# Kernel tuning notes

Hardware: AMD Instinct MI355X
Metric: run time of the kernel (lower is better)

## Reference

```python
import jax, jax.numpy as jnp
import numpy as np

INPUT_SIZE = 40960
HIDDEN = 256
BATCH = 16384
FEATS_PER_SAMPLE = 32


def _bag_sum(W, idx, offsets, num_segments):
    # EmbeddingBag(mode='sum'): segment ids from CSR offsets
    seg = jnp.searchsorted(offsets, jnp.arange(idx.shape[0]), side='right') - 1
    return jax.ops.segment_sum(W[idx], seg, num_segments=num_segments)


def setup_inputs() -> dict:
    key = jax.random.key(0)
    ks = jax.random.split(key, 12)
    n = BATCH * FEATS_PER_SAMPLE
    white_indices = jax.random.randint(ks[0], (n,), 0, INPUT_SIZE)
    black_indices = jax.random.randint(ks[1], (n,), 0, INPUT_SIZE)
    offsets = jnp.arange(BATCH, dtype=jnp.int64) * FEATS_PER_SAMPLE
    stm = (jax.random.uniform(ks[2], (BATCH, 1)) > 0.5).astype(jnp.float32)
    s_ft = 1.0 / np.sqrt(HIDDEN)
    ft_w = jax.random.uniform(ks[3], (INPUT_SIZE, HIDDEN), minval=-s_ft, maxval=s_ft)
    ft_b = jnp.zeros((HIDDEN,), jnp.float32)
    s1 = 1.0 / np.sqrt(2 * HIDDEN)
    l1_w = jax.random.uniform(ks[4], (32, 2 * HIDDEN), minval=-s1, maxval=s1)
    l1_b = jax.random.uniform(ks[5], (32,), minval=-s1, maxval=s1)
    s2 = 1.0 / np.sqrt(32)
    l2_w = jax.random.uniform(ks[6], (32, 32), minval=-s2, maxval=s2)
    l2_b = jax.random.uniform(ks[7], (32,), minval=-s2, maxval=s2)
    l3_w = jax.random.uniform(ks[8], (1, 32), minval=-s2, maxval=s2)
    l3_b = jax.random.uniform(ks[9], (1,), minval=-s2, maxval=s2)
    return {
        'white_indices': white_indices, 'white_offsets': offsets,
        'black_indices': black_indices, 'black_offsets': offsets,
        'stm': stm,
        'ft_w': ft_w, 'ft_b': ft_b,
        'l1_w': l1_w, 'l1_b': l1_b,
        'l2_w': l2_w, 'l2_b': l2_b,
        'l3_w': l3_w, 'l3_b': l3_b,
    }


def reference(white_indices, white_offsets, black_indices, black_offsets, stm,
              ft_w, ft_b, l1_w, l1_b, l2_w, l2_b, l3_w, l3_b):
    B = stm.shape[0]
    wh = jnp.clip(_bag_sum(ft_w, white_indices, white_offsets, B) + ft_b, 0.0, 1.0)
    bh = jnp.clip(_bag_sum(ft_w, black_indices, black_offsets, B) + ft_b, 0.0, 1.0)
    stm_b = stm.astype(bool)  # (B,1)
    hidden = jnp.where(stm_b,
                       jnp.concatenate([wh, bh], axis=-1),
                       jnp.concatenate([bh, wh], axis=-1))  # (B, 512)
    x = jnp.clip(hidden @ l1_w.T + l1_b, 0.0, 1.0)
    x = jnp.clip(x @ l2_w.T + l2_b, 0.0, 1.0)
    return x @ l3_w.T + l3_b  # (B, 1)
```

## Files before the change

### kernel.cpp

```cpp
#include <hip/hip_runtime.h>
#include <hip/hip_bf16.h>

#define NBATCH 16384
#define WPB 4
#define BLOCK 256

typedef unsigned int u32;
typedef unsigned char u8;

#define ENC 2032.0f
#define DEC 4.92125984e-4f
#define BIAS_SUM (4096.0f * DEC)

__device__ __forceinline__ float clamp01(float x){ return fminf(fmaxf(x, 0.f), 1.f); }

template<int D>
__device__ __forceinline__ float lane_xor_f(float x) {
    if constexpr (D == 1)
        return __int_as_float(__builtin_amdgcn_update_dpp(
            0, __float_as_int(x), 0xB1 , 0xF, 0xF, true));
    else if constexpr (D == 2)
        return __int_as_float(__builtin_amdgcn_update_dpp(
            0, __float_as_int(x), 0x4E , 0xF, 0xF, true));
    else
        return __shfl_xor(x, D, 64);
}

template<int D>
__device__ __forceinline__ void rs_stage(float (&p)[32], int lane) {
    const int mb = lane & D;
    #pragma unroll
    for (int j = 0; j < D; ++j) {
        float a = p[j], b = p[j + D];
        float snd = mb ? a : b;
        float kp  = mb ? b : a;
        p[j] = kp + lane_xor_f<D>(snd);
    }
}

__global__ __launch_bounds__(256) void convert_ftw_u8(
    const float* __restrict__ src, u32* __restrict__ dst, int n4)
{
    int i = blockIdx.x * blockDim.x + threadIdx.x;
    const int stride = gridDim.x * blockDim.x;
    for (; i < n4; i += stride) {
        float4 v = ((const float4*)src)[i];
        int q0 = __float2int_rn(v.x * ENC) + 128;
        int q1 = __float2int_rn(v.y * ENC) + 128;
        int q2 = __float2int_rn(v.z * ENC) + 128;
        int q3 = __float2int_rn(v.w * ENC) + 128;
        q0 = max(0, min(255, q0)); q1 = max(0, min(255, q1));
        q2 = max(0, min(255, q2)); q3 = max(0, min(255, q3));
        dst[i] = (u32)q0 | ((u32)q1 << 8) | ((u32)q2 << 16) | ((u32)q3 << 24);
    }
}

__global__ __launch_bounds__(BLOCK, 4) void nnue_fwd_u8tab(
    const int* __restrict__ wi, const int* __restrict__ bi,
    const float* __restrict__ stm,
    const u8* __restrict__ tab, const float* __restrict__ ftb,
    const float* __restrict__ l1w, const float* __restrict__ l1b,
    const float* __restrict__ l2w, const float* __restrict__ l2b,
    const float* __restrict__ l3w, const float* __restrict__ l3b,
    float* __restrict__ out)
{
    __shared__ __align__(16) float l1w_s[16*512];
    __shared__ __align__(16) float x1_s[WPB][32];
    __shared__ int idx_s[WPB][64];

    const int tid  = threadIdx.x;
    const int lane = tid & 63;
    const int wv   = tid >> 6;
    const int s    = blockIdx.x * WPB + wv;

    {
        const float4* src = (const float4*)l1w;
        #pragma unroll
        for (int i = 0; i < 8; ++i) {
            int j = tid + i*BLOCK;
            int B = j * 16;
            int W = B ^ ((B >> 3) & 16);
            *(float4*)((char*)l1w_s + W) = src[j];
        }
    }
    {
        int bse = s*32 + (lane & 31);
        idx_s[wv][lane] = (lane < 32) ? wi[bse] : bi[bse];
    }
    const bool wf = stm[s] > 0.5f;
    __syncthreads();

    const int chunk = lane & 31;
    const int hsel  = lane & 32;

    u32 sA = 0, sB = 0, sC = 0, sD = 0;
    #pragma unroll 8
    for (int j = 0; j < 32; ++j) {
        int row = idx_s[wv][j + hsel];
        uint2 w = *(const uint2*)(tab + (size_t)row*256 + chunk*8);
        sA += (w.x      ) & 0x00FF00FFu;
        sB += (w.x >> 8 ) & 0x00FF00FFu;
        sC += (w.y      ) & 0x00FF00FFu;
        sD += (w.y >> 8 ) & 0x00FF00FFu;
    }
    float acc[8];
    {
        float4 a = *(const float4*)(ftb + chunk*8);
        float4 b = *(const float4*)(ftb + chunk*8 + 4);
        acc[0] = fmaf((float)(sA & 0xFFFFu), DEC, a.x - BIAS_SUM);
        acc[1] = fmaf((float)(sB & 0xFFFFu), DEC, a.y - BIAS_SUM);
        acc[2] = fmaf((float)(sA >> 16    ), DEC, a.z - BIAS_SUM);
        acc[3] = fmaf((float)(sB >> 16    ), DEC, a.w - BIAS_SUM);
        acc[4] = fmaf((float)(sC & 0xFFFFu), DEC, b.x - BIAS_SUM);
        acc[5] = fmaf((float)(sD & 0xFFFFu), DEC, b.y - BIAS_SUM);
        acc[6] = fmaf((float)(sC >> 16    ), DEC, b.z - BIAS_SUM);
        acc[7] = fmaf((float)(sD >> 16    ), DEC, b.w - BIAS_SUM);
    }
    #pragma unroll
    for (int k = 0; k < 8; ++k) acc[k] = clamp01(acc[k]);

    const int wl    = wf ? lane : (lane ^ 32);
    const int wbyte = wl * 32;

    float p[32];
    #pragma unroll
    for (int o = 0; o < 16; ++o) {
        int b  = o*2048 + wbyte;
        int sw = b ^ ((b >> 3) & 16);
        float4 wa = *(const float4*)((const char*)l1w_s + sw);
        float4 wb = *(const float4*)((const char*)l1w_s + (sw ^ 16));
        p[o] = acc[0]*wa.x + acc[1]*wa.y + acc[2]*wa.z + acc[3]*wa.w
             + acc[4]*wb.x + acc[5]*wb.y + acc[6]*wb.z + acc[7]*wb.w;
    }
    __syncthreads();

    {
        const float4* src = (const float4*)l1w;
        #pragma unroll
        for (int i = 0; i < 8; ++i) {
            int j = tid + i*BLOCK;
            int B = j * 16;
            int W = B ^ ((B >> 3) & 16);
            *(float4*)((char*)l1w_s + W) = src[2048 + j];
        }
    }
    __syncthreads();

    const int j2 = lane & 31;
    float4 w2[8];
    {
        const float4* l2p = (const float4*)(l2w + j2*32);
        #pragma unroll
        for (int i = 0; i < 8; ++i) w2[i] = l2p[i];
    }
    const float l1b_r = l1b[j2];
    const float l2b_r = l2b[j2];
    const float l3w_r = l3w[j2];

    #pragma unroll
    for (int o = 0; o < 16; ++o) {
        int b  = o*2048 + wbyte;
        int sw = b ^ ((b >> 3) & 16);
        float4 wa = *(const float4*)((const char*)l1w_s + sw);
        float4 wb = *(const float4*)((const char*)l1w_s + (sw ^ 16));
        p[16+o] = acc[0]*wa.x + acc[1]*wa.y + acc[2]*wa.z + acc[3]*wa.w
                + acc[4]*wb.x + acc[5]*wb.y + acc[6]*wb.z + acc[7]*wb.w;
    }

    rs_stage<16>(p, lane);
    rs_stage<8 >(p, lane);
    rs_stage<4 >(p, lane);
    rs_stage<2 >(p, lane);
    rs_stage<1 >(p, lane);
    float psum = p[0] + __shfl_xor(p[0], 32, 64);

    float x1 = clamp01(psum + l1b_r);
    if (lane < 32) x1_s[wv][lane] = x1;

    const float4* xs = (const float4*)x1_s[wv];
    float a2 = l2b_r;
    #pragma unroll
    for (int i = 0; i < 8; ++i) {
        float4 xv = xs[i];
        a2 += xv.x*w2[i].x + xv.y*w2[i].y + xv.z*w2[i].z + xv.w*w2[i].w;
    }
    float x2 = clamp01(a2);

    float r = x2 * l3w_r;
    #pragma unroll
    for (int d = 16; d >= 1; d >>= 1) r += __shfl_xor(r, d, 64);

    if (lane == 0) out[s] = r + l3b[0];
}

__global__ __launch_bounds__(256, 4) void nnue_fwd_f32(
    const int* __restrict__ wi, const int* __restrict__ bi,
    const float* __restrict__ stm,
    const float* __restrict__ ftw, const float* __restrict__ ftb,
    const float* __restrict__ l1w, const float* __restrict__ l1b,
    const float* __restrict__ l2w, const float* __restrict__ l2b,
    const float* __restrict__ l3w, const float* __restrict__ l3b,
    float* __restrict__ out)
{
    __shared__ __align__(16) float l1w_s[16*512];
    __shared__ float l2w_s[32*33];
    __shared__ float l1b_s[32], l2b_s[32], l3w_s[32];
    __shared__ int idx_s[4][64];

    const int tid  = threadIdx.x;
    const int lane = tid & 63;
    const int wv   = tid >> 6;
    const int s    = blockIdx.x * 4 + wv;

    {
        const float4* src = (const float4*)l1w;
        float4* dst = (float4*)l1w_s;
        #pragma unroll
        for (int i = 0; i < 8; ++i) dst[tid + i*256] = src[tid + i*256];
    }
    for (int i = tid; i < 1024; i += 256)
        l2w_s[(i >> 5)*33 + (i & 31)] = l2w[i];
    if (tid < 32) {
        l1b_s[tid] = l1b[tid];
        l2b_s[tid] = l2b[tid];
        l3w_s[tid] = l3w[tid];
    }
    {
        int bse = s*32 + (lane & 31);
        idx_s[wv][lane] = (lane < 32) ? wi[bse] : bi[bse];
    }
    __syncthreads();

    const int chunk = lane & 31;
    const int hsel  = lane & 32;

    float acc[8];
    {
        float4 a = *(const float4*)(ftb + chunk*8);
        float4 b = *(const float4*)(ftb + chunk*8 + 4);
        acc[0]=a.x; acc[1]=a.y; acc[2]=a.z; acc[3]=a.w;
        acc[4]=b.x; acc[5]=b.y; acc[6]=b.z; acc[7]=b.w;
    }
    #pragma unroll 8
    for (int j = 0; j < 32; ++j) {
        int row = idx_s[wv][j + hsel];
        const float* rp = ftw + (size_t)row*256 + chunk*8;
        float4 a = *(const float4*)rp;
        float4 b = *(const float4*)(rp + 4);
        acc[0]+=a.x; acc[1]+=a.y; acc[2]+=a.z; acc[3]+=a.w;
        acc[4]+=b.x; acc[5]+=b.y; acc[6]+=b.z; acc[7]+=b.w;
    }
    #pragma unroll
    for (int k = 0; k < 8; ++k) acc[k] = clamp01(acc[k]);

    const bool wf = stm[s] > 0.5f;
    float h[8];
    #pragma unroll
    for (int k = 0; k < 8; ++k) {
        float x = __shfl_xor(acc[k], 32, 64);
        h[k] = wf ? acc[k] : x;
    }

    float p[32];
    #pragma unroll
    for (int o = 0; o < 16; ++o) {
        float4 wa = *(const float4*)&l1w_s[o*512 + lane*8];
        float4 wb = *(const float4*)&l1w_s[o*512 + lane*8 + 4];
        p[o] = h[0]*wa.x + h[1]*wa.y + h[2]*wa.z + h[3]*wa.w
             + h[4]*wb.x + h[5]*wb.y + h[6]*wb.z + h[7]*wb.w;
    }
    __syncthreads();
    {
        const float4* src = (const float4*)l1w;
        float4* dst = (float4*)l1w_s;
        #pragma unroll
        for (int i = 0; i < 8; ++i) dst[tid + i*256] = src[2048 + tid + i*256];
    }
    __syncthreads();
    #pragma unroll
    for (int o = 0; o < 16; ++o) {
        float4 wa = *(const float4*)&l1w_s[o*512 + lane*8];
        float4 wb = *(const float4*)&l1w_s[o*512 + lane*8 + 4];
        p[16+o] = h[0]*wa.x + h[1]*wa.y + h[2]*wa.z + h[3]*wa.w
                + h[4]*wb.x + h[5]*wb.y + h[6]*wb.z + h[7]*wb.w;
    }
    #pragma unroll
    for (int o = 0; o < 32; ++o) {
        #pragma unroll
        for (int d = 1; d < 64; d <<= 1)
            p[o] += __shfl_xor(p[o], d, 64);
    }
    float x1[32];
    #pragma unroll
    for (int o = 0; o < 32; ++o) x1[o] = clamp01(p[o] + l1b_s[o]);

    const int j2 = lane & 31;
    float a2 = l2b_s[j2];
    #pragma unroll
    for (int i = 0; i < 32; ++i) a2 += x1[i] * l2w_s[j2*33 + i];
    float x2 = clamp01(a2);

    float r = x2 * l3w_s[j2];
    #pragma unroll
    for (int d = 16; d >= 1; d >>= 1) r += __shfl_xor(r, d, 64);

    if (lane == 0) out[s] = r + l3b[0];
}

extern "C" void kernel_launch(void* const* d_in, const int* in_sizes, int n_in,
                              void* d_out, int out_size, void* d_ws, size_t ws_size,
                              hipStream_t stream)
{
    const int*   wi  = (const int*)d_in[0];
    const int*   bi  = (const int*)d_in[2];
    const float* stm = (const float*)d_in[4];
    const float* ftw = (const float*)d_in[5];
    const float* ftb = (const float*)d_in[6];
    const float* l1w = (const float*)d_in[7];
    const float* l1b = (const float*)d_in[8];
    const float* l2w = (const float*)d_in[9];
    const float* l2b = (const float*)d_in[10];
    const float* l3w = (const float*)d_in[11];
    const float* l3b = (const float*)d_in[12];

    const size_t tab_elems = (size_t)40960 * 256;
    const size_t need = tab_elems * sizeof(u8);
    if (ws_size >= need) {
        u8* tab = (u8*)d_ws;
        convert_ftw_u8<<<dim3(4096), dim3(256), 0, stream>>>(
            ftw, (u32*)tab, (int)(tab_elems / 4));
        nnue_fwd_u8tab<<<dim3(NBATCH / WPB), dim3(BLOCK), 0, stream>>>(
            wi, bi, stm, tab, ftb, l1w, l1b, l2w, l2b, l3w, l3b,
            (float*)d_out);
    } else {
        nnue_fwd_f32<<<dim3(NBATCH / 4), dim3(256), 0, stream>>>(
            wi, bi, stm, ftw, ftb, l1w, l1b, l2w, l2b, l3w, l3b,
            (float*)d_out);
    }
}
```

Before: 156.4 us.

## Halve L1 weight LDS tile and stage in four passes for higher occupancy

The shared l1 weight buffer shrinks from 32KB to 16KB and is refilled in four passes of 8 outputs instead of two passes of 16. Launch bounds rise to 8 blocks per CU. The layer-2 weights are no longer held in registers but read lazily from global memory, and the gather address math is simplified to 32-bit. This targets more resident waves to hide gather latency, at the cost of extra barriers and global reloads of l1 weights per block.

```diff
diff --git a/kernel.cpp b/kernel.cpp
--- a/kernel.cpp
+++ b/kernel.cpp
@@ -55,7 +55,7 @@
     }
 }
 
-__global__ __launch_bounds__(BLOCK, 4) void nnue_fwd_u8tab(
+__global__ __launch_bounds__(BLOCK, 8) void nnue_fwd_u8tab(
     const int* __restrict__ wi, const int* __restrict__ bi,
     const float* __restrict__ stm,
     const u8* __restrict__ tab, const float* __restrict__ ftb,
@@ -64,7 +64,7 @@
     const float* __restrict__ l3w, const float* __restrict__ l3b,
     float* __restrict__ out)
 {
-    __shared__ __align__(16) float l1w_s[16*512];
+    __shared__ __align__(16) float l1w_s[8*512];
     __shared__ __align__(16) float x1_s[WPB][32];
     __shared__ int idx_s[WPB][64];
 
@@ -76,11 +76,10 @@
     {
         const float4* src = (const float4*)l1w;
         #pragma unroll
-        for (int i = 0; i < 8; ++i) {
+        for (int i = 0; i < 4; ++i) {
             int j = tid + i*BLOCK;
             int B = j * 16;
-            int W = B ^ ((B >> 3) & 16);
-            *(float4*)((char*)l1w_s + W) = src[j];
+            *(float4*)((char*)l1w_s + (B ^ ((B >> 3) & 16))) = src[j];
         }
     }
     {
@@ -92,12 +91,13 @@
 
     const int chunk = lane & 31;
     const int hsel  = lane & 32;
+    const u32 coff  = (u32)chunk * 8u;
 
     u32 sA = 0, sB = 0, sC = 0, sD = 0;
     #pragma unroll 8
     for (int j = 0; j < 32; ++j) {
-        int row = idx_s[wv][j + hsel];
-        uint2 w = *(const uint2*)(tab + (size_t)row*256 + chunk*8);
+        u32 row = (u32)idx_s[wv][j + hsel];
+        uint2 w = *(const uint2*)(tab + ((row << 8) + coff));
         sA += (w.x      ) & 0x00FF00FFu;
         sB += (w.x >> 8 ) & 0x00FF00FFu;
         sC += (w.y      ) & 0x00FF00FFu;
@@ -121,51 +121,42 @@
 
     const int wl    = wf ? lane : (lane ^ 32);
     const int wbyte = wl * 32;
+    const int swb   = wbyte ^ ((wbyte >> 3) & 16);
+    const char* lbase  = (const char*)l1w_s + swb;
+    const char* lbase2 = (const char*)l1w_s + (swb ^ 16);
 
     float p[32];
     #pragma unroll
-    for (int o = 0; o < 16; ++o) {
-        int b  = o*2048 + wbyte;
-        int sw = b ^ ((b >> 3) & 16);
-        float4 wa = *(const float4*)((const char*)l1w_s + sw);
-        float4 wb = *(const float4*)((const char*)l1w_s + (sw ^ 16));
-        p[o] = acc[0]*wa.x + acc[1]*wa.y + acc[2]*wa.z + acc[3]*wa.w
-             + acc[4]*wb.x + acc[5]*wb.y + acc[6]*wb.z + acc[7]*wb.w;
-    }
-    __syncthreads();
-
-    {
-        const float4* src = (const float4*)l1w;
-        #pragma unroll
-        for (int i = 0; i < 8; ++i) {
-            int j = tid + i*BLOCK;
-            int B = j * 16;
-            int W = B ^ ((B >> 3) & 16);
-            *(float4*)((char*)l1w_s + W) = src[2048 + j];
+    for (int ol = 0; ol < 8; ++ol) {
+        float4 wa = *(const float4*)(lbase  + ol*2048);
+        float4 wb = *(const float4*)(lbase2 + ol*2048);
+        p[ol] = acc[0]*wa.x + acc[1]*wa.y + acc[2]*wa.z + acc[3]*wa.w
+              + acc[4]*wb.x + acc[5]*wb.y + acc[6]*wb.z + acc[7]*wb.w;
+    }
+    #pragma unroll
+    for (int pass = 1; pass < 4; ++pass) {
+        __syncthreads();
+        {
+            const float4* src = (const float4*)l1w + pass*1024;
+            #pragma unroll
+            for (int i = 0; i < 4; ++i) {
+                int j = tid + i*BLOCK;
+                int B = j * 16;
+                *(float4*)((char*)l1w_s + (B ^ ((B >> 3) & 16))) = src[j];
+            }
         }
-    }
-    __syncthreads();
+        __syncthreads();
+        #pragma unroll
+        for (int ol = 0; ol < 8; ++ol) {
+            float4 wa = *(const float4*)(lbase  + ol*2048);
+            float4 wb = *(const float4*)(lbase2 + ol*2048);
+            p[pass*8+ol] = acc[0]*wa.x + acc[1]*wa.y + acc[2]*wa.z + acc[3]*wa.w
+                         + acc[4]*wb.x + acc[5]*wb.y + acc[6]*wb.z + acc[7]*wb.w;
+        }
+    }
 
     const int j2 = lane & 31;
-    float4 w2[8];
-    {
-        const float4* l2p = (const float4*)(l2w + j2*32);
-        #pragma unroll
-        for (int i = 0; i < 8; ++i) w2[i] = l2p[i];
-    }
     const float l1b_r = l1b[j2];
-    const float l2b_r = l2b[j2];
-    const float l3w_r = l3w[j2];
-
-    #pragma unroll
-    for (int o = 0; o < 16; ++o) {
-        int b  = o*2048 + wbyte;
-        int sw = b ^ ((b >> 3) & 16);
-        float4 wa = *(const float4*)((const char*)l1w_s + sw);
-        float4 wb = *(const float4*)((const char*)l1w_s + (sw ^ 16));
-        p[16+o] = acc[0]*wa.x + acc[1]*wa.y + acc[2]*wa.z + acc[3]*wa.w
-                + acc[4]*wb.x + acc[5]*wb.y + acc[6]*wb.z + acc[7]*wb.w;
-    }
 
     rs_stage<16>(p, lane);
     rs_stage<8 >(p, lane);
@@ -177,16 +168,18 @@
     float x1 = clamp01(psum + l1b_r);
     if (lane < 32) x1_s[wv][lane] = x1;
 
-    const float4* xs = (const float4*)x1_s[wv];
-    float a2 = l2b_r;
+    const float4* xs  = (const float4*)x1_s[wv];
+    const float4* l2p = (const float4*)(l2w + j2*32);
+    float a2 = l2b[j2];
     #pragma unroll
     for (int i = 0; i < 8; ++i) {
-        float4 xv = xs[i];
-        a2 += xv.x*w2[i].x + xv.y*w2[i].y + xv.z*w2[i].z + xv.w*w2[i].w;
+        float4 wv2 = l2p[i];
+        float4 xv  = xs[i];
+        a2 += xv.x*wv2.x + xv.y*wv2.y + xv.z*wv2.z + xv.w*wv2.w;
     }
     float x2 = clamp01(a2);
 
-    float r = x2 * l3w_r;
+    float r = x2 * l3w[j2];
     #pragma unroll
     for (int d = 16; d >= 1; d >>= 1) r += __shfl_xor(r, d, 64);
 
```

New measurement: 154.7 us. No clear change (-1.1%).
